# Performance work log

Hardware: AMD Instinct MI355X
Metric: run time of the kernel (lower is better)

## Reference

```python
import jax, jax.numpy as jnp
import numpy as np

N_NODES = 100000
N_EDGES = 2000000
N_GRAPHS = 1000
DIM = 32
NUM_FEATURES = 7
NUM_CLASSES = 2
BN_EPS = 1e-5


def setup_inputs() -> dict:
    key = jax.random.key(0)
    ks = jax.random.split(key, 24)
    inp = {
        "x": jax.random.normal(ks[0], (N_NODES, NUM_FEATURES), dtype=jnp.float32),
        "edge_index": jax.random.randint(ks[1], (2, N_EDGES), 0, N_NODES, dtype=jnp.int64),
        "batch": jnp.sort(jax.random.randint(ks[2], (N_NODES,), 0, N_GRAPHS, dtype=jnp.int64)),
        "conv1_W1": jax.random.normal(ks[3], (NUM_FEATURES, DIM), dtype=jnp.float32) * 0.3,
        "conv1_b1": jax.random.normal(ks[4], (DIM,), dtype=jnp.float32) * 0.1,
        "conv1_W2": jax.random.normal(ks[5], (DIM, DIM), dtype=jnp.float32) * 0.15,
        "conv1_b2": jax.random.normal(ks[6], (DIM,), dtype=jnp.float32) * 0.1,
        "convs_W1": jax.random.normal(ks[7], (4, DIM, DIM), dtype=jnp.float32) * 0.15,
        "convs_b1": jax.random.normal(ks[8], (4, DIM), dtype=jnp.float32) * 0.1,
        "convs_W2": jax.random.normal(ks[9], (4, DIM, DIM), dtype=jnp.float32) * 0.15,
        "convs_b2": jax.random.normal(ks[10], (4, DIM), dtype=jnp.float32) * 0.1,
        "bn_gamma": jax.random.uniform(ks[11], (5, DIM), dtype=jnp.float32, minval=0.5, maxval=1.5),
        "bn_beta": jax.random.normal(ks[12], (5, DIM), dtype=jnp.float32) * 0.1,
        "bn_mean": jax.random.normal(ks[13], (5, DIM), dtype=jnp.float32) * 0.1,
        "bn_var": jax.random.uniform(ks[14], (5, DIM), dtype=jnp.float32, minval=0.5, maxval=1.5),
        "fc1_W": jax.random.normal(ks[15], (DIM, DIM), dtype=jnp.float32) * 0.15,
        "fc1_b": jax.random.normal(ks[16], (DIM,), dtype=jnp.float32) * 0.1,
        "fc2_W": jax.random.normal(ks[17], (DIM, NUM_CLASSES), dtype=jnp.float32) * 0.15,
        "fc2_b": jax.random.normal(ks[18], (NUM_CLASSES,), dtype=jnp.float32) * 0.1,
    }
    return inp


def _gin_conv(h, src, dst, W1, b1, W2, b2):
    # GINConv with eps=0: nn((1+eps)*x + sum_{j in N(i)} x_j)
    agg = jax.ops.segment_sum(h[src], dst, num_segments=N_NODES)
    z = h + agg
    z = jnp.maximum(z @ W1 + b1, 0.0)
    return z @ W2 + b2


def _bn_eval(h, gamma, beta, mean, var):
    return (h - mean) * jax.lax.rsqrt(var + BN_EPS) * gamma + beta


def reference(x, edge_index, batch,
              conv1_W1, conv1_b1, conv1_W2, conv1_b2,
              convs_W1, convs_b1, convs_W2, convs_b2,
              bn_gamma, bn_beta, bn_mean, bn_var,
              fc1_W, fc1_b, fc2_W, fc2_b):
    src, dst = edge_index[0], edge_index[1]
    h = _gin_conv(x, src, dst, conv1_W1, conv1_b1, conv1_W2, conv1_b2)
    h = jnp.maximum(h, 0.0)
    h = _bn_eval(h, bn_gamma[0], bn_beta[0], bn_mean[0], bn_var[0])
    for i in range(4):  # conv2..conv5
        h = _gin_conv(h, src, dst, convs_W1[i], convs_b1[i], convs_W2[i], convs_b2[i])
        h = jnp.maximum(h, 0.0)
        h = _bn_eval(h, bn_gamma[i + 1], bn_beta[i + 1], bn_mean[i + 1], bn_var[i + 1])
    # global add pool over graphs
    g = jax.ops.segment_sum(h, batch, num_segments=N_GRAPHS)  # [G, DIM]
    g = jnp.maximum(g @ fc1_W + fc1_b, 0.0)
    # dropout: eval mode -> identity
    logits = g @ fc2_W + fc2_b
    return jax.nn.log_softmax(logits, axis=-1)
```

## Files before the change

kernel.cpp:

```cpp
#include <hip/hip_runtime.h>

#define N_NODES  100000
#define N_EDGES  2000000
#define N_GRAPHS 1000
#define NFEAT    7
#define BN_EPS   1e-5f
#define MAXDEG   64

#define BSH      7
#define NBKT     782
#define BCAP     3584
#define E_PER_BLK 4096
#define NGRP     6250

__device__ __forceinline__ unsigned bf16_rne(float f) {
  unsigned u = __float_as_uint(f);
  return (u + 0x7FFFu + ((u >> 16) & 1u)) >> 16;
}
__device__ __forceinline__ float bf_lo(unsigned u) { return __uint_as_float(u << 16); }
__device__ __forceinline__ float bf_hi(unsigned u) { return __uint_as_float(u & 0xFFFF0000u); }

typedef __bf16 bf16x8 __attribute__((ext_vector_type(8)));
typedef float  f32x4  __attribute__((ext_vector_type(4)));

__global__ __launch_bounds__(1024) void b1_bucket(const int* __restrict__ src,
                                                  const int* __restrict__ dst,
                                                  int* __restrict__ gCur,
                                                  unsigned* __restrict__ ebuf) {
  __shared__ int hist[NBKT], base[NBKT];
  int tid = threadIdx.x;
  for (int i = tid; i < NBKT; i += 1024) hist[i] = 0;
  __syncthreads();
  unsigned pk[4];
  int bo[4];
  int e0 = blockIdx.x * E_PER_BLK;
#pragma unroll
  for (int k = 0; k < 4; ++k) {
    int e = e0 + k * 1024 + tid;
    if (e < N_EDGES) {
      int d = dst[e], s = src[e];
      int b = d >> BSH;
      int off = atomicAdd(&hist[b], 1);
      pk[k] = ((unsigned)(d & 127) << 17) | (unsigned)s;
      bo[k] = (b << 17) | off;
    } else {
      bo[k] = -1;
    }
  }
  __syncthreads();
  for (int i = tid; i < NBKT; i += 1024)
    base[i] = hist[i] ? atomicAdd(&gCur[i], hist[i]) : 0;
  __syncthreads();
#pragma unroll
  for (int k = 0; k < 4; ++k) {
    if (bo[k] >= 0) {
      int b = bo[k] >> 17, off = bo[k] & 0x1FFFF;
      int p = base[b] + off;
      if (p < BCAP) ebuf[(size_t)b * BCAP + p] = pk[k];
    }
  }
}

__global__ __launch_bounds__(512) void b2_csr(const unsigned* __restrict__ ebuf,
                                              const int* __restrict__ gCnt,
                                              int* __restrict__ cnt,
                                              int* __restrict__ csr,
                                              int* __restrict__ gmax) {
  __shared__ int hist[128];
  __shared__ int stage[128 * MAXDEG];
  int b = blockIdx.x, tid = threadIdx.x;
  if (tid < 128) hist[tid] = 0;
  for (int i = tid; i < 128 * MAXDEG; i += 512) stage[i] = (b << BSH) + (i >> 6);
  __syncthreads();
  int n = gCnt[b];
  if (n > BCAP) n = BCAP;
  const unsigned* eb = ebuf + (size_t)b * BCAP;
  for (int i = tid; i < n; i += 512) {
    unsigned pk = eb[i];
    int dloc = (int)(pk >> 17);
    int slot = atomicAdd(&hist[dloc], 1);
    if (slot < MAXDEG) stage[(dloc << 6) + slot] = (int)(pk & 0x1FFFFu);
  }
  __syncthreads();
  if (tid < 128) {
    int gnode = (b << BSH) + tid;
    if (gnode < N_NODES) cnt[gnode] = hist[tid];
  }
  if (tid < 8) {
    int mx = 1;
#pragma unroll
    for (int k = 0; k < 16; ++k) {
      int d = hist[tid * 16 + k];
      if (d > 63) d = 63;
      if (d + 1 > mx) mx = d + 1;
    }
    gmax[(b << 3) + tid] = mx;
  }
  const int4* st4 = (const int4*)stage;
  int4* dst4 = (int4*)(csr + (size_t)b * (128 * MAXDEG));
  for (int i = tid; i < 128 * MAXDEG / 4; i += 512) dst4[i] = st4[i];
}

__global__ __launch_bounds__(256) void xcvt_kernel(const float* __restrict__ x,
                                                   unsigned* __restrict__ xc) {
  int i = blockIdx.x * 256 + threadIdx.x;
  if (i >= N_NODES * 4) return;
  int n = i >> 2, p = i & 3;
  float lo = x[n * 7 + 2 * p];
  float hi = (2 * p + 1 < 7) ? x[n * 7 + 2 * p + 1] : 0.f;
  xc[i] = bf16_rne(lo) | (bf16_rne(hi) << 16);
}

__global__ __launch_bounds__(256) void gin1(
    const unsigned short* __restrict__ xc16, const int* __restrict__ cnt,
    const int* __restrict__ csr, const int* __restrict__ gmax,
    const float* __restrict__ W1, const float* __restrict__ b1,
    const float* __restrict__ W2, const float* __restrict__ b2,
    const float* __restrict__ gamma, const float* __restrict__ beta,
    const float* __restrict__ mean, const float* __restrict__ var,
    unsigned short* __restrict__ hout16) {
  __shared__ __align__(16) float zs[4][16][12];
  __shared__ __align__(16) float ts[4][16][36];
  int tid = threadIdx.x;
  int w = __builtin_amdgcn_readfirstlane(tid >> 6);
  int lane = tid & 63;
  int nl = lane & 15;
  int q  = lane >> 4;

  bf16x8 w1ah, w1al, w1bh, w1bl;
#pragma unroll
  for (int i = 0; i < 8; ++i) {
    float fa = 0.f, fb = 0.f;
    if (q == 0 && i < 7) {
      fa = W1[i * 32 + nl];
      fb = W1[i * 32 + 16 + nl];
    }
    __bf16 ha = (__bf16)fa;
    w1ah[i] = ha; w1al[i] = (__bf16)(fa - (float)ha);
    __bf16 hb = (__bf16)fb;
    w1bh[i] = hb; w1bl[i] = (__bf16)(fb - (float)hb);
  }
  bf16x8 w2ah, w2al, w2bh, w2bl;
#pragma unroll
  for (int i = 0; i < 8; ++i) {
    float f;
    __bf16 h;
    f = W2[(q * 8 + i) * 32 + nl];       h = (__bf16)f;
    w2ah[i] = h; w2al[i] = (__bf16)(f - (float)h);
    f = W2[(q * 8 + i) * 32 + 16 + nl];  h = (__bf16)f;
    w2bh[i] = h; w2bl[i] = (__bf16)(f - (float)h);
  }
  float vb1a = b1[nl], vb1b = b1[16 + nl];
  float vb2a = b2[nl], vb2b = b2[16 + nl];
  f32x4 cb1a = {vb1a, vb1a, vb1a, vb1a};
  f32x4 cb1b = {vb1b, vb1b, vb1b, vb1b};
  f32x4 cb2a = {vb2a, vb2a, vb2a, vb2a};
  f32x4 cb2b = {vb2b, vb2b, vb2b, vb2b};
  float sc0 = gamma[nl] * rsqrtf(var[nl] + BN_EPS);
  float sh0 = beta[nl] - mean[nl] * sc0;
  float sc1 = gamma[16 + nl] * rsqrtf(var[16 + nl] + BN_EPS);
  float sh1 = beta[16 + nl] - mean[16 + nl] * sc1;

  const unsigned* xc32 = (const unsigned*)xc16;

  const int NW = gridDim.x * 4;
  for (int g = blockIdx.x * 4 + w; g < NGRP; g += NW) {
    int node = g * 16 + nl;
    int dcnt = cnt[node];
    if (dcnt > 63) dcnt = 63;
    int dE = dcnt + 1;
    int dmax = __builtin_amdgcn_readfirstlane(gmax[g]);
    int nb = (dmax + 3) >> 2;

    const int* crow = csr + (size_t)node * MAXDEG;
    float a0 = 0.f, a1 = 0.f;

    uint4 iA = *(const uint4*)crow;
    unsigned r0 = xc32[(size_t)iA.x * 4 + q];
    unsigned r1 = xc32[(size_t)iA.y * 4 + q];
    unsigned r2 = xc32[(size_t)iA.z * 4 + q];
    unsigned r3 = xc32[(size_t)iA.w * 4 + q];
    uint4 iB = iA;
    if (nb > 1) iB = *(const uint4*)(crow + 4);

    for (int b = 0; b < nb; ++b) {
      bool hasN = (b + 1 < nb);
      unsigned n0 = r0, n1 = r1, n2 = r2, n3 = r3;
      if (hasN) {
        n0 = xc32[(size_t)iB.x * 4 + q];
        n1 = xc32[(size_t)iB.y * 4 + q];
        n2 = xc32[(size_t)iB.z * 4 + q];
        n3 = xc32[(size_t)iB.w * 4 + q];
      }
      uint4 iC = iB;
      if (b + 2 < nb) iC = *(const uint4*)(crow + (b + 2) * 4);

      int s0 = b * 4;
      if (s0 + 0 < dE) { a0 += bf_lo(r0); a1 += bf_hi(r0); }
      if (s0 + 1 < dE) { a0 += bf_lo(r1); a1 += bf_hi(r1); }
      if (s0 + 2 < dE) { a0 += bf_lo(r2); a1 += bf_hi(r2); }
      if (s0 + 3 < dE) { a0 += bf_lo(r3); a1 += bf_hi(r3); }
      r0 = n0; r1 = n1; r2 = n2; r3 = n3;
      iB = iC;
    }

    {
      float2 z0 = {a0, a1};
      *(float2*)&zs[w][nl][q * 2] = z0;
    }
    bf16x8 af, afl;
#pragma unroll
    for (int i = 0; i < 8; ++i) { af[i] = (__bf16)0.f; afl[i] = (__bf16)0.f; }
    if (q == 0) {
      float4 z0 = *(const float4*)&zs[w][nl][0];
      float4 z1 = *(const float4*)&zs[w][nl][4];
      float zv[8] = {z0.x, z0.y, z0.z, z0.w, z1.x, z1.y, z1.z, z1.w};
#pragma unroll
      for (int i = 0; i < 8; ++i) {
        __bf16 h = (__bf16)zv[i];
        af[i] = h;
        afl[i] = (__bf16)(zv[i] - (float)h);
      }
    }

    f32x4 t0 = __builtin_amdgcn_mfma_f32_16x16x32_bf16(af,  w1ah, cb1a, 0, 0, 0);
    t0 = __builtin_amdgcn_mfma_f32_16x16x32_bf16(afl, w1ah, t0, 0, 0, 0);
    t0 = __builtin_amdgcn_mfma_f32_16x16x32_bf16(af,  w1al, t0, 0, 0, 0);
    f32x4 t1 = __builtin_amdgcn_mfma_f32_16x16x32_bf16(af,  w1bh, cb1b, 0, 0, 0);
    t1 = __builtin_amdgcn_mfma_f32_16x16x32_bf16(afl, w1bh, t1, 0, 0, 0);
    t1 = __builtin_amdgcn_mfma_f32_16x16x32_bf16(af,  w1bl, t1, 0, 0, 0);
#pragma unroll
    for (int r = 0; r < 4; ++r) {
      t0[r] = fmaxf(t0[r], 0.f);
      t1[r] = fmaxf(t1[r], 0.f);
    }
#pragma unroll
    for (int r = 0; r < 4; ++r) {
      ts[w][q * 4 + r][nl]      = t0[r];
      ts[w][q * 4 + r][16 + nl] = t1[r];
    }
    bf16x8 af2, af2l;
    {
      float4 r0f = *(const float4*)&ts[w][nl][q * 8];
      float4 r1f = *(const float4*)&ts[w][nl][q * 8 + 4];
      float tv[8] = {r0f.x, r0f.y, r0f.z, r0f.w, r1f.x, r1f.y, r1f.z, r1f.w};
#pragma unroll
      for (int i = 0; i < 8; ++i) {
        __bf16 h = (__bf16)tv[i];
        af2[i] = h;
        af2l[i] = (__bf16)(tv[i] - (float)h);
      }
    }

    f32x4 o0 = __builtin_amdgcn_mfma_f32_16x16x32_bf16(af2,  w2ah, cb2a, 0, 0, 0);
    o0 = __builtin_amdgcn_mfma_f32_16x16x32_bf16(af2l, w2ah, o0, 0, 0, 0);
    o0 = __builtin_amdgcn_mfma_f32_16x16x32_bf16(af2,  w2al, o0, 0, 0, 0);
    f32x4 o1 = __builtin_amdgcn_mfma_f32_16x16x32_bf16(af2,  w2bh, cb2b, 0, 0, 0);
    o1 = __builtin_amdgcn_mfma_f32_16x16x32_bf16(af2l, w2bh, o1, 0, 0, 0);
    o1 = __builtin_amdgcn_mfma_f32_16x16x32_bf16(af2,  w2bl, o1, 0, 0, 0);
#pragma unroll
    for (int r = 0; r < 4; ++r) {
      o0[r] = fmaxf(o0[r], 0.f) * sc0 + sh0;
      o1[r] = fmaxf(o1[r], 0.f) * sc1 + sh1;
    }
#pragma unroll
    for (int r = 0; r < 4; ++r) {
      ts[w][q * 4 + r][nl]      = o0[r];
      ts[w][q * 4 + r][16 + nl] = o1[r];
    }
    {
      float4 f0 = *(const float4*)&ts[w][nl][q * 8];
      float4 f1 = *(const float4*)&ts[w][nl][q * 8 + 4];
      uint4 st;
      st.x = bf16_rne(f0.x) | (bf16_rne(f0.y) << 16);
      st.y = bf16_rne(f0.z) | (bf16_rne(f0.w) << 16);
      st.z = bf16_rne(f1.x) | (bf16_rne(f1.y) << 16);
      st.w = bf16_rne(f1.z) | (bf16_rne(f1.w) << 16);
      *(uint4*)(hout16 + (size_t)node * 32 + q * 8) = st;
    }
  }
}

__global__ __launch_bounds__(256) void gin_layer32(
    const unsigned short* __restrict__ hin16, const int* __restrict__ cnt,
    const int* __restrict__ csr, const int* __restrict__ gmax,
    const float* __restrict__ W1, const float* __restrict__ b1,
    const float* __restrict__ W2, const float* __restrict__ b2,
    const float* __restrict__ gamma, const float* __restrict__ beta,
    const float* __restrict__ mean, const float* __restrict__ var,
    unsigned short* __restrict__ hout16) {
  __shared__ __align__(16) float ts[4][16][36];
  int tid = threadIdx.x;
  int w = __builtin_amdgcn_readfirstlane(tid >> 6);
  int lane = tid & 63;
  int nl = lane & 15;
  int q  = lane >> 4;

  bf16x8 w1ah, w1al, w1bh, w1bl, w2ah, w2al, w2bh, w2bl;
#pragma unroll
  for (int i = 0; i < 8; ++i) {
    float f;
    __bf16 h;
    f = W1[(q * 8 + i) * 32 + nl];       h = (__bf16)f;
    w1ah[i] = h; w1al[i] = (__bf16)(f - (float)h);
    f = W1[(q * 8 + i) * 32 + 16 + nl];  h = (__bf16)f;
    w1bh[i] = h; w1bl[i] = (__bf16)(f - (float)h);
    f = W2[(q * 8 + i) * 32 + nl];       h = (__bf16)f;
    w2ah[i] = h; w2al[i] = (__bf16)(f - (float)h);
    f = W2[(q * 8 + i) * 32 + 16 + nl];  h = (__bf16)f;
    w2bh[i] = h; w2bl[i] = (__bf16)(f - (float)h);
  }
  float vb1a = b1[nl], vb1b = b1[16 + nl];
  float vb2a = b2[nl], vb2b = b2[16 + nl];
  f32x4 cb1a = {vb1a, vb1a, vb1a, vb1a};
  f32x4 cb1b = {vb1b, vb1b, vb1b, vb1b};
  f32x4 cb2a = {vb2a, vb2a, vb2a, vb2a};
  f32x4 cb2b = {vb2b, vb2b, vb2b, vb2b};
  float sc0 = gamma[nl] * rsqrtf(var[nl] + BN_EPS);
  float sh0 = beta[nl] - mean[nl] * sc0;
  float sc1 = gamma[16 + nl] * rsqrtf(var[16 + nl] + BN_EPS);
  float sh1 = beta[16 + nl] - mean[16 + nl] * sc1;

  const int NW = gridDim.x * 4;
  for (int g = blockIdx.x * 4 + w; g < NGRP; g += NW) {
    int node = g * 16 + nl;
    int dcnt = cnt[node];
    if (dcnt > 63) dcnt = 63;
    int dE = dcnt + 1;
    int dmax = __builtin_amdgcn_readfirstlane(gmax[g]);
    int nb = (dmax + 3) >> 2;

    const int* crow = csr + (size_t)node * MAXDEG;
    float acc[8];
#pragma unroll
    for (int i = 0; i < 8; ++i) acc[i] = 0.f;

    uint4 iA = *(const uint4*)crow;
    uint4 r0 = *(const uint4*)(hin16 + (size_t)iA.x * 32 + q * 8);
    uint4 r1 = *(const uint4*)(hin16 + (size_t)iA.y * 32 + q * 8);
    uint4 r2 = *(const uint4*)(hin16 + (size_t)iA.z * 32 + q * 8);
    uint4 r3 = *(const uint4*)(hin16 + (size_t)iA.w * 32 + q * 8);
    uint4 iB = iA;
    if (nb > 1) iB = *(const uint4*)(crow + 4);

    for (int b = 0; b < nb; ++b) {
      bool hasN = (b + 1 < nb);
      uint4 n0 = r0, n1 = r1, n2 = r2, n3 = r3;
      if (hasN) {
        n0 = *(const uint4*)(hin16 + (size_t)iB.x * 32 + q * 8);
        n1 = *(const uint4*)(hin16 + (size_t)iB.y * 32 + q * 8);
        n2 = *(const uint4*)(hin16 + (size_t)iB.z * 32 + q * 8);
        n3 = *(const uint4*)(hin16 + (size_t)iB.w * 32 + q * 8);
      }
      uint4 iC = iB;
      if (b + 2 < nb) iC = *(const uint4*)(crow + (b + 2) * 4);

      int s0 = b * 4;
      if (s0 + 0 < dE) {
        acc[0] += bf_lo(r0.x); acc[1] += bf_hi(r0.x);
        acc[2] += bf_lo(r0.y); acc[3] += bf_hi(r0.y);
        acc[4] += bf_lo(r0.z); acc[5] += bf_hi(r0.z);
        acc[6] += bf_lo(r0.w); acc[7] += bf_hi(r0.w);
      }
      if (s0 + 1 < dE) {
        acc[0] += bf_lo(r1.x); acc[1] += bf_hi(r1.x);
        acc[2] += bf_lo(r1.y); acc[3] += bf_hi(r1.y);
        acc[4] += bf_lo(r1.z); acc[5] += bf_hi(r1.z);
        acc[6] += bf_lo(r1.w); acc[7] += bf_hi(r1.w);
      }
      if (s0 + 2 < dE) {
        acc[0] += bf_lo(r2.x); acc[1] += bf_hi(r2.x);
        acc[2] += bf_lo(r2.y); acc[3] += bf_hi(r2.y);
        acc[4] += bf_lo(r2.z); acc[5] += bf_hi(r2.z);
        acc[6] += bf_lo(r2.w); acc[7] += bf_hi(r2.w);
      }
      if (s0 + 3 < dE) {
        acc[0] += bf_lo(r3.x); acc[1] += bf_hi(r3.x);
        acc[2] += bf_lo(r3.y); acc[3] += bf_hi(r3.y);
        acc[4] += bf_lo(r3.z); acc[5] += bf_hi(r3.z);
        acc[6] += bf_lo(r3.w); acc[7] += bf_hi(r3.w);
      }
      r0 = n0; r1 = n1; r2 = n2; r3 = n3;
      iB = iC;
    }

    bf16x8 af, afl;
#pragma unroll
    for (int i = 0; i < 8; ++i) {
      __bf16 h = (__bf16)acc[i];
      af[i] = h;
      afl[i] = (__bf16)(acc[i] - (float)h);
    }

    f32x4 t0 = __builtin_amdgcn_mfma_f32_16x16x32_bf16(af,  w1ah, cb1a, 0, 0, 0);
    t0 = __builtin_amdgcn_mfma_f32_16x16x32_bf16(afl, w1ah, t0, 0, 0, 0);
    t0 = __builtin_amdgcn_mfma_f32_16x16x32_bf16(af,  w1al, t0, 0, 0, 0);
    f32x4 t1 = __builtin_amdgcn_mfma_f32_16x16x32_bf16(af,  w1bh, cb1b, 0, 0, 0);
    t1 = __builtin_amdgcn_mfma_f32_16x16x32_bf16(afl, w1bh, t1, 0, 0, 0);
    t1 = __builtin_amdgcn_mfma_f32_16x16x32_bf16(af,  w1bl, t1, 0, 0, 0);
#pragma unroll
    for (int r = 0; r < 4; ++r) {
      t0[r] = fmaxf(t0[r], 0.f);
      t1[r] = fmaxf(t1[r], 0.f);
    }
#pragma unroll
    for (int r = 0; r < 4; ++r) {
      ts[w][q * 4 + r][nl]      = t0[r];
      ts[w][q * 4 + r][16 + nl] = t1[r];
    }
    bf16x8 af2, af2l;
    {
      float4 r0f = *(const float4*)&ts[w][nl][q * 8];
      float4 r1f = *(const float4*)&ts[w][nl][q * 8 + 4];
      float tv[8] = {r0f.x, r0f.y, r0f.z, r0f.w, r1f.x, r1f.y, r1f.z, r1f.w};
#pragma unroll
      for (int i = 0; i < 8; ++i) {
        __bf16 h = (__bf16)tv[i];
        af2[i] = h;
        af2l[i] = (__bf16)(tv[i] - (float)h);
      }
    }

    f32x4 o0 = __builtin_amdgcn_mfma_f32_16x16x32_bf16(af2,  w2ah, cb2a, 0, 0, 0);
    o0 = __builtin_amdgcn_mfma_f32_16x16x32_bf16(af2l, w2ah, o0, 0, 0, 0);
    o0 = __builtin_amdgcn_mfma_f32_16x16x32_bf16(af2,  w2al, o0, 0, 0, 0);
    f32x4 o1 = __builtin_amdgcn_mfma_f32_16x16x32_bf16(af2,  w2bh, cb2b, 0, 0, 0);
    o1 = __builtin_amdgcn_mfma_f32_16x16x32_bf16(af2l, w2bh, o1, 0, 0, 0);
    o1 = __builtin_amdgcn_mfma_f32_16x16x32_bf16(af2,  w2bl, o1, 0, 0, 0);
#pragma unroll
    for (int r = 0; r < 4; ++r) {
      o0[r] = fmaxf(o0[r], 0.f) * sc0 + sh0;
      o1[r] = fmaxf(o1[r], 0.f) * sc1 + sh1;
    }
#pragma unroll
    for (int r = 0; r < 4; ++r) {
      ts[w][q * 4 + r][nl]      = o0[r];
      ts[w][q * 4 + r][16 + nl] = o1[r];
    }
    {
      float4 f0 = *(const float4*)&ts[w][nl][q * 8];
      float4 f1 = *(const float4*)&ts[w][nl][q * 8 + 4];
      uint4 st;
      st.x = bf16_rne(f0.x) | (bf16_rne(f0.y) << 16);
      st.y = bf16_rne(f0.z) | (bf16_rne(f0.w) << 16);
      st.z = bf16_rne(f1.x) | (bf16_rne(f1.y) << 16);
      st.w = bf16_rne(f1.z) | (bf16_rne(f1.w) << 16);
      *(uint4*)(hout16 + (size_t)node * 32 + q * 8) = st;
    }
  }
}

__global__ __launch_bounds__(256) void pool_kernel(const unsigned short* __restrict__ h16,
                                                   const int* __restrict__ batch,
                                                   float* __restrict__ g) {
  __shared__ int s_lo, s_hi;
  __shared__ float red[8][33];
  int gr = blockIdx.x;
  if (threadIdx.x == 0) {
    int lo = 0, hi = N_NODES;
    while (lo < hi) { int m = (lo + hi) >> 1; if (batch[m] < gr) lo = m + 1; else hi = m; }
    s_lo = lo;
  } else if (threadIdx.x == 1) {
    int lo = 0, hi = N_NODES;
    while (lo < hi) { int m = (lo + hi) >> 1; if (batch[m] < gr + 1) lo = m + 1; else hi = m; }
    s_hi = lo;
  }
  __syncthreads();
  int lo = s_lo, hi = s_hi;
  int j = threadIdx.x & 31;
  int nd = threadIdx.x >> 5;
  float acc = 0.f;
  for (int n = lo + nd; n < hi; n += 8)
    acc += __uint_as_float((unsigned)h16[n * 32 + j] << 16);
  red[nd][j] = acc;
  __syncthreads();
  if (threadIdx.x < 32) {
    float s = 0.f;
#pragma unroll
    for (int r = 0; r < 8; ++r) s += red[r][j];
    g[gr * 32 + j] = s;
  }
}

__global__ __launch_bounds__(256) void head_kernel(
    const float* __restrict__ g, const float* __restrict__ W1, const float* __restrict__ b1,
    const float* __restrict__ W2, const float* __restrict__ b2, float* __restrict__ out) {
  __shared__ float sW1[1024], sb1[32];
  __shared__ float sW2[64], sb2[2];
  __shared__ float zb[8][33], tb[8][33], lb[8][2];
  int tid = threadIdx.x;
  for (int i = tid; i < 1024; i += 256) sW1[i] = W1[i];
  if (tid < 64) sW2[tid] = W2[tid];
  if (tid < 32) sb1[tid] = b1[tid];
  if (tid < 2) sb2[tid] = b2[tid];
  int nd = tid >> 5;
  int gr = blockIdx.x * 8 + nd;
  int j = tid & 31;
  __syncthreads();
  float z = (gr < N_GRAPHS) ? g[gr * 32 + j] : 0.f;
  zb[nd][j] = z;
  __syncthreads();
  float t = sb1[j];
#pragma unroll
  for (int k = 0; k < 32; ++k) t = fmaf(zb[nd][k], sW1[k * 32 + j], t);
  t = fmaxf(t, 0.f);
  tb[nd][j] = t;
  __syncthreads();
  if (j < 2) {
    float l = sb2[j];
#pragma unroll
    for (int k = 0; k < 32; ++k) l = fmaf(tb[nd][k], sW2[k * 2 + j], l);
    lb[nd][j] = l;
  }
  __syncthreads();
  if (gr < N_GRAPHS && j < 2) {
    float l0 = lb[nd][0], l1 = lb[nd][1];
    float m = fmaxf(l0, l1);
    float lse = m + logf(expf(l0 - m) + expf(l1 - m));
    out[gr * 2 + j] = lb[nd][j] - lse;
  }
}

extern "C" void kernel_launch(void* const* d_in, const int* in_sizes, int n_in,
                              void* d_out, int out_size, void* d_ws, size_t ws_size,
                              hipStream_t stream) {
  const float* x     = (const float*)d_in[0];
  const int*   eidx  = (const int*)d_in[1];
  const int*   batch = (const int*)d_in[2];
  const float* c1W1  = (const float*)d_in[3];
  const float* c1b1  = (const float*)d_in[4];
  const float* c1W2  = (const float*)d_in[5];
  const float* c1b2  = (const float*)d_in[6];
  const float* csW1  = (const float*)d_in[7];
  const float* csb1  = (const float*)d_in[8];
  const float* csW2  = (const float*)d_in[9];
  const float* csb2  = (const float*)d_in[10];
  const float* bng   = (const float*)d_in[11];
  const float* bnb   = (const float*)d_in[12];
  const float* bnm   = (const float*)d_in[13];
  const float* bnv   = (const float*)d_in[14];
  const float* fc1W  = (const float*)d_in[15];
  const float* fc1b  = (const float*)d_in[16];
  const float* fc2W  = (const float*)d_in[17];
  const float* fc2b  = (const float*)d_in[18];
  float* out = (float*)d_out;

  const int* src = eidx;
  const int* dst = eidx + N_EDGES;

  char* p = (char*)d_ws;
  unsigned short* hA16 = (unsigned short*)p; p += (size_t)N_NODES * 32 * 2;
  unsigned short* hB16 = (unsigned short*)p; p += (size_t)N_NODES * 32 * 2;
  int*      cnt  = (int*)p;      p += (size_t)N_NODES * 4;
  int*      csr  = (int*)p;      p += (size_t)NBKT * 128 * MAXDEG * 4;
  unsigned* ebuf = (unsigned*)p; p += (size_t)NBKT * BCAP * 4;
  int*      gCur = (int*)p;      p += 1024 * 4;
  int*      gmax = (int*)p;      p += (size_t)(NBKT * 8) * 4;
  float*    g    = (float*)p;    p += (size_t)N_GRAPHS * 32 * 4;
  unsigned* xc = ebuf;

  (void)hipMemsetAsync(gCur, 0, 1024 * 4, stream);
  b1_bucket<<<(N_EDGES + E_PER_BLK - 1) / E_PER_BLK, 1024, 0, stream>>>(src, dst, gCur, ebuf);
  b2_csr<<<NBKT, 512, 0, stream>>>(ebuf, gCur, cnt, csr, gmax);

  xcvt_kernel<<<(N_NODES * 4 + 255) / 256, 256, 0, stream>>>(x, xc);

  gin1<<<(NGRP + 3) / 4, 256, 0, stream>>>(
      (const unsigned short*)xc, cnt, csr, gmax, c1W1, c1b1, c1W2, c1b2,
      bng, bnb, bnm, bnv, hA16);

  unsigned short* cur = hA16;
  unsigned short* nxt = hB16;
  for (int i = 0; i < 4; ++i) {
    gin_layer32<<<(NGRP + 3) / 4, 256, 0, stream>>>(
        cur, cnt, csr, gmax,
        csW1 + (size_t)i * 1024, csb1 + (size_t)i * 32,
        csW2 + (size_t)i * 1024, csb2 + (size_t)i * 32,
        bng + (size_t)(i + 1) * 32, bnb + (size_t)(i + 1) * 32,
        bnm + (size_t)(i + 1) * 32, bnv + (size_t)(i + 1) * 32, nxt);
    unsigned short* tmp = cur; cur = nxt; nxt = tmp;
  }

  pool_kernel<<<N_GRAPHS, 256, 0, stream>>>(cur, batch, g);
  head_kernel<<<(N_GRAPHS + 7) / 8, 256, 0, stream>>>(g, fc1W, fc1b, fc2W, fc2b, out);
}
```

Measured before the change: 293.4 us.

## Sort nodes by degree within buckets to cut per-group neighbor loop padding

Within each 128-node bucket, nodes are counting-sorted by descending degree and a node permutation is written out. The GIN layer kernels process 16-node groups through this permutation, so each group's max degree, which sets the wavefront's neighbor-loop trip count, tracks the actual degrees more closely and fewer padded iterations run. The cost is an extra indirection load per node, scattered rather than contiguous output writes and CSR row reads, and more shared-memory work in the CSR build kernel.

```diff
diff --git a/kernel.cpp b/kernel.cpp
--- a/kernel.cpp
+++ b/kernel.cpp
@@ -65,11 +65,15 @@
                                               const int* __restrict__ gCnt,
                                               int* __restrict__ cnt,
                                               int* __restrict__ csr,
+                                              int* __restrict__ order,
                                               int* __restrict__ gmax) {
   __shared__ int hist[128];
   __shared__ int stage[128 * MAXDEG];
+  __shared__ int dEs[128], keyof[128], order_s[128];
+  __shared__ int binBase[64], binFill[64];
   int b = blockIdx.x, tid = threadIdx.x;
   if (tid < 128) hist[tid] = 0;
+  if (tid >= 128 && tid < 192) binFill[tid - 128] = 0;
   for (int i = tid; i < 128 * MAXDEG; i += 512) stage[i] = (b << BSH) + (i >> 6);
   __syncthreads();
   int n = gCnt[b];
@@ -84,17 +88,46 @@
   __syncthreads();
   if (tid < 128) {
     int gnode = (b << BSH) + tid;
-    if (gnode < N_NODES) cnt[gnode] = hist[tid];
+    bool valid = gnode < N_NODES;
+    int d = hist[tid];
+    if (d > 63) d = 63;
+    int dE = d + 1;
+    dEs[tid] = valid ? dE : 0;
+    if (valid) cnt[gnode] = hist[tid];
+    int key = valid ? (64 - dE) : 9999;
+    keyof[tid] = key;
+    if (valid) atomicAdd(&binFill[key], 1);
+  }
+  __syncthreads();
+  if (tid == 0) {
+    int s = 0;
+#pragma unroll
+    for (int k2 = 0; k2 < 64; ++k2) { binBase[k2] = s; s += binFill[k2]; }
+  }
+  __syncthreads();
+  if (tid < 64) binFill[tid] = 0;
+  __syncthreads();
+  if (tid < 128 && keyof[tid] < 64) {
+    int pos = binBase[keyof[tid]] + atomicAdd(&binFill[keyof[tid]], 1);
+    order_s[pos] = tid;
+  }
+  __syncthreads();
+  if (tid < 128) {
+    int gpos = b * 128 + tid;
+    if (gpos < N_NODES) order[gpos] = (b << BSH) + order_s[tid];
   }
   if (tid < 8) {
-    int mx = 1;
-#pragma unroll
-    for (int k = 0; k < 16; ++k) {
-      int d = hist[tid * 16 + k];
-      if (d > 63) d = 63;
-      if (d + 1 > mx) mx = d + 1;
-    }
-    gmax[(b << 3) + tid] = mx;
+    int nv = N_NODES - (b << BSH);
+    if (nv > 128) nv = 128;
+    if (tid * 16 < nv) {
+      int mx = 1;
+#pragma unroll
+      for (int k = 0; k < 16; ++k) {
+        int dv = dEs[order_s[tid * 16 + k]];
+        if (dv > mx) mx = dv;
+      }
+      gmax[(b << 3) + tid] = mx;
+    }
   }
   const int4* st4 = (const int4*)stage;
   int4* dst4 = (int4*)(csr + (size_t)b * (128 * MAXDEG));
@@ -113,7 +146,8 @@
 
 __global__ __launch_bounds__(256) void gin1(
     const unsigned short* __restrict__ xc16, const int* __restrict__ cnt,
-    const int* __restrict__ csr, const int* __restrict__ gmax,
+    const int* __restrict__ csr, const int* __restrict__ order,
+    const int* __restrict__ gmax,
     const float* __restrict__ W1, const float* __restrict__ b1,
     const float* __restrict__ W2, const float* __restrict__ b2,
     const float* __restrict__ gamma, const float* __restrict__ beta,
@@ -165,7 +199,7 @@
 
   const int NW = gridDim.x * 4;
   for (int g = blockIdx.x * 4 + w; g < NGRP; g += NW) {
-    int node = g * 16 + nl;
+    int node = order[g * 16 + nl];
     int dcnt = cnt[node];
     if (dcnt > 63) dcnt = 63;
     int dE = dcnt + 1;
@@ -283,7 +317,8 @@
 
 __global__ __launch_bounds__(256) void gin_layer32(
     const unsigned short* __restrict__ hin16, const int* __restrict__ cnt,
-    const int* __restrict__ csr, const int* __restrict__ gmax,
+    const int* __restrict__ csr, const int* __restrict__ order,
+    const int* __restrict__ gmax,
     const float* __restrict__ W1, const float* __restrict__ b1,
     const float* __restrict__ W2, const float* __restrict__ b2,
     const float* __restrict__ gamma, const float* __restrict__ beta,
@@ -323,7 +358,7 @@
 
   const int NW = gridDim.x * 4;
   for (int g = blockIdx.x * 4 + w; g < NGRP; g += NW) {
-    int node = g * 16 + nl;
+    int node = order[g * 16 + nl];
     int dcnt = cnt[node];
     if (dcnt > 63) dcnt = 63;
     int dE = dcnt + 1;
@@ -556,24 +591,25 @@
   unsigned* ebuf = (unsigned*)p; p += (size_t)NBKT * BCAP * 4;
   int*      gCur = (int*)p;      p += 1024 * 4;
   int*      gmax = (int*)p;      p += (size_t)(NBKT * 8) * 4;
+  int*      order = (int*)p;     p += (size_t)(NBKT * 128) * 4;
   float*    g    = (float*)p;    p += (size_t)N_GRAPHS * 32 * 4;
   unsigned* xc = ebuf;
 
   (void)hipMemsetAsync(gCur, 0, 1024 * 4, stream);
   b1_bucket<<<(N_EDGES + E_PER_BLK - 1) / E_PER_BLK, 1024, 0, stream>>>(src, dst, gCur, ebuf);
-  b2_csr<<<NBKT, 512, 0, stream>>>(ebuf, gCur, cnt, csr, gmax);
+  b2_csr<<<NBKT, 512, 0, stream>>>(ebuf, gCur, cnt, csr, order, gmax);
 
   xcvt_kernel<<<(N_NODES * 4 + 255) / 256, 256, 0, stream>>>(x, xc);
 
   gin1<<<(NGRP + 3) / 4, 256, 0, stream>>>(
-      (const unsigned short*)xc, cnt, csr, gmax, c1W1, c1b1, c1W2, c1b2,
+      (const unsigned short*)xc, cnt, csr, order, gmax, c1W1, c1b1, c1W2, c1b2,
       bng, bnb, bnm, bnv, hA16);
 
   unsigned short* cur = hA16;
   unsigned short* nxt = hB16;
   for (int i = 0; i < 4; ++i) {
     gin_layer32<<<(NGRP + 3) / 4, 256, 0, stream>>>(
-        cur, cnt, csr, gmax,
+        cur, cnt, csr, order, gmax,
         csW1 + (size_t)i * 1024, csb1 + (size_t)i * 32,
         csW2 + (size_t)i * 1024, csb2 + (size_t)i * 32,
         bng + (size_t)(i + 1) * 32, bnb + (size_t)(i + 1) * 32,
```

Result: slower. 301.5 us (+2.7%).
